# Kernel tuning notes

Measured on AMD Instinct MI355X. Metric: run time of the kernel, lower is better.

The kernel has to match this reference:

```python
import jax, jax.numpy as jnp
import numpy as np

M, N, P, T = 8000, 63, 64, 5


def setup_inputs() -> dict:
    key = jax.random.key(0)
    ks = jax.random.split(key, 19)
    sn = (1.0 / N) ** 0.5
    sp = (1.0 / P) ** 0.5
    f32 = jnp.float32
    return {
        "A": jax.random.normal(ks[0], (1, M, N), f32),
        "b": jax.random.normal(ks[1], (1, M), f32),
        "c": jax.random.normal(ks[2], (1, N), f32),
        "theta1r": sn * jax.random.normal(ks[3], (P, N + 1), f32),
        "theta1c": sn * jax.random.normal(ks[4], (P, N + 1), f32),
        "theta2rr": sp * jax.random.normal(ks[5], (P, P), f32),
        "theta2rc": sp * jax.random.normal(ks[6], (P, P), f32),
        "theta2cr": sp * jax.random.normal(ks[7], (P, P), f32),
        "theta3rr": sp * jax.random.normal(ks[8], (P, P), f32),
        "theta3rc": sp * jax.random.normal(ks[9], (P, P), f32),
        "theta3cr": sp * jax.random.normal(ks[10], (P, P), f32),
        "theta4rr": sp * jax.random.normal(ks[11], (P,), f32),
        "theta4rc": sp * jax.random.normal(ks[12], (P,), f32),
        "theta4cr": sp * jax.random.normal(ks[13], (P,), f32),
        "theta6r": sp * jax.random.normal(ks[14], (P, P), f32),
        "theta6c": sp * jax.random.normal(ks[15], (P, P), f32),
        "theta7": sp * jax.random.normal(ks[16], (P, P), f32),
        "W8": 0.05 * jax.random.normal(ks[17], (2, 2 * P), f32),
        "b8": 0.05 * jax.random.normal(ks[18], (2,), f32),
        "z": 7,
    }


def reference(A, b, c, theta1r, theta1c, theta2rr, theta2rc, theta2cr,
              theta3rr, theta3rc, theta3cr, theta4rr, theta4rc, theta4cr,
              theta6r, theta6c, theta7, W8, b8, z):
    relu = jax.nn.relu
    m, n = A.shape[1], A.shape[2]
    p = theta1r.shape[0]
    # raw node features: row node v -> [A[v,:], b[v]]; column node m -> [c, 0]
    Fr_raw = jnp.concatenate([A[0], b[0][:, None]], axis=1)        # (m, n+1)
    fc_raw = jnp.concatenate([c[0], jnp.zeros((1,), A.dtype)])     # (n+1,)
    Fr = Fr_raw / jnp.linalg.norm(Fr_raw, axis=1, keepdims=True)   # f(v), v < m
    fc = fc_raw / jnp.linalg.norm(fc_raw)                          # f(m)
    # edge weights w(v,u) = f(v).f(u) are detached in the original (float(...data))
    Frd = jax.lax.stop_gradient(Fr)
    fcd = jax.lax.stop_gradient(fc)
    Wrr = Frd @ Frd.T                                              # (m, m)
    dg = jnp.diagonal(Wrr)
    srr_pos = relu(Wrr).sum(axis=1) - relu(dg)                     # sum over u != v
    srr_neg = relu(-Wrr).sum(axis=1) - relu(-dg)
    wrc = Frd @ fcd                                                # (m,) = w(v, m)
    # identity: sum_u relu(t4 * w_u) = relu(t4) * sum_u relu(w_u) + relu(-t4) * sum_u relu(-w_u)
    Srr = relu(theta4rr)[:, None] * srr_pos[None, :] + relu(-theta4rr)[:, None] * srr_neg[None, :]
    Src = relu(theta4rc)[:, None] * relu(wrc)[None, :] + relu(-theta4rc)[:, None] * relu(-wrc)[None, :]
    scr = relu(theta4cr) * relu(wrc).sum() + relu(-theta4cr) * relu(-wrc).sum()
    edge_r = theta3rr @ Srr + theta3rc @ Src                       # (p, m), constant over t
    edge_c = theta3cr @ scr                                        # (p,)
    fz = Fr[z]                                                     # z < m: row node feature
    t1r = theta1r @ fz                                             # (p,)
    t1c = theta1c @ fz
    # mu init (p, m+1) = [[Ab^T, c0^T]; 0]; split into row columns / column node
    mu_r0 = jnp.zeros((p, m), A.dtype).at[: n + 1].set(Fr_raw.T)
    mu_c0 = jnp.zeros((p,), A.dtype).at[: n + 1].set(fc_raw)

    def step(carry, _):
        mu_r, mu_c = carry
        # row nodes: term2rr uses old mu[:, v]; term2rc uses old mu[:, m]
        new_r = relu(t1r[:, None] + theta2rr @ mu_r + (theta2rc @ mu_c)[:, None] + edge_r)
        # column node updated last within a sweep -> sees updated row embeddings
        new_c = relu(t1c + theta2cr @ new_r.sum(axis=1) + edge_c)
        return (new_r, new_c), None

    (mu_r, mu_c), _ = jax.lax.scan(step, (mu_r0, mu_c0), None, length=T)
    term6 = theta6r @ mu_r.sum(axis=1) + theta6c @ mu_c            # (p,)
    term7 = theta7 @ mu_r[:, z]                                    # (p,)
    feat = jax.nn.sigmoid(jnp.concatenate([term6, term7]))         # (2p,)
    return (feat @ W8.T + b8)[None, :]                             # (1, 2)
```

## Files before the change

### kernel.cpp

```cpp
#include <hip/hip_runtime.h>
#include <math.h>

typedef __attribute__((ext_vector_type(8))) short short8;
typedef __attribute__((ext_vector_type(4))) float f32x4;

#define WS_SPART 0
#define WS_GPART 131072
#define WS_WPART 163840
#define WS_CPART 164864
#define WS_T1R   204864
#define WS_T1C   204928
#define WS_AL    204992
#define WS_BE    205056
#define WS_GA    205120
#define WS_DE    205184
#define WS_ECP   205248
#define WS_ECN   205312
#define WS_W     205376
#define WS_MUZ   205760
#define WS_WSUM  205824
#define WS_RNORM 205888
#define WS_R2H   214080
#define WS_R2L   216128
#define WS_E4    218176
#define WS_FH    250176
#define WS_FL    512320

__device__ __forceinline__ float waveReduceSum(float v) {
#pragma unroll
    for (int m = 32; m >= 1; m >>= 1) v += __shfl_xor(v, m, 64);
    return v;
}
__device__ __forceinline__ unsigned short f2bf(float f) {
    unsigned int u = __float_as_uint(f);
    unsigned int r = (u + 0x7fffu + ((u >> 16) & 1u)) >> 16;
    return (unsigned short)r;
}
__device__ __forceinline__ float bf2f(unsigned short h) {
    return __uint_as_float(((unsigned int)h) << 16);
}

__global__ __launch_bounds__(256) void k_fr(
    const float* __restrict__ A, const float* __restrict__ b, const float* __restrict__ c,
    const float* __restrict__ th1r, const float* __restrict__ th1c,
    const float* __restrict__ th2rr, const float* __restrict__ th2rc,
    const float* __restrict__ th3rr, const float* __restrict__ th3rc, const float* __restrict__ th3cr,
    const float* __restrict__ th4rr, const float* __restrict__ th4rc, const float* __restrict__ th4cr,
    const int* __restrict__ zp,
    unsigned short* __restrict__ Fh, unsigned short* __restrict__ Fl,
    unsigned short* __restrict__ R2H, unsigned short* __restrict__ R2L,
    float* __restrict__ ws)
{
    int tid = threadIdx.x, lane = tid & 63, wid = tid >> 6;

    if (blockIdx.x == 512) {
        __shared__ float fcraw[64], fz[64], sh4a[64], sh4b[64];
        int p = lane;
        int z = zp[0];
        float cv = (p < 63) ? c[p] : 0.f;
        fcraw[p] = cv;
        float av = (p < 63) ? A[z * 63 + p] : b[z];
        float s2 = waveReduceSum(av * av);
        fz[p] = av * rsqrtf(s2);
        __syncthreads();

        float t1 = 0.f, t2 = 0.f, w0 = 0.f;
#pragma unroll 8
        for (int k = 0; k < 64; k++) {
            t1 += th1r[p * 64 + k] * fz[k];
            t2 += th1c[p * 64 + k] * fz[k];
            w0 += th2rc[p * 64 + k] * fcraw[k];
        }
        ws[WS_T1R + p] = t1;
        ws[WS_T1C + p] = t2;
        ws[WS_W + p] = t1 + w0;

        sh4a[p] = th4rr[p];
        sh4b[p] = th4rc[p];
        __syncthreads();
        float a = 0.f, bb = 0.f, g = 0.f, d = 0.f;
#pragma unroll 8
        for (int k = 0; k < 64; k++) {
            float t4 = sh4a[k];
            a  += th3rr[p * 64 + k] * fmaxf(t4, 0.f);
            bb += th3rr[p * 64 + k] * fmaxf(-t4, 0.f);
            float t5 = sh4b[k];
            g  += th3rc[p * 64 + k] * fmaxf(t5, 0.f);
            d  += th3rc[p * 64 + k] * fmaxf(-t5, 0.f);
        }
        ws[WS_AL + p] = a; ws[WS_BE + p] = bb;
        ws[WS_GA + p] = g; ws[WS_DE + p] = d;
        __syncthreads();
        sh4a[p] = th4cr[p];
        __syncthreads();
        float e1 = 0.f, e2 = 0.f;
#pragma unroll 8
        for (int k = 0; k < 64; k++) {
            float t6 = sh4a[k];
            e1 += th3cr[p * 64 + k] * fmaxf(t6, 0.f);
            e2 += th3cr[p * 64 + k] * fmaxf(-t6, 0.f);
        }
        ws[WS_ECP + p] = e1; ws[WS_ECN + p] = e2;

#pragma unroll
        for (int i = 0; i < 16; i++) {
            int idx = tid * 16 + i;
            float f = th2rr[idx];
            unsigned short h = f2bf(f);
            R2H[idx] = h;
            R2L[idx] = f2bf(f - bf2f(h));
        }
        return;
    }

    __shared__ float gsh[64];
    __shared__ float wsh2[2];
    if (tid < 64) gsh[tid] = 0.f;
    if (tid < 2) wsh2[tid] = 0.f;
    __syncthreads();

    float cv = (lane < 63) ? c[lane] : 0.f;
    float cn2 = waveReduceSum(cv * cv);
    float fcnl = cv * rsqrtf(cn2);

    int r0 = blockIdx.x * 16 + wid * 4;
    float gl = 0.f, lp = 0.f, ln = 0.f;
#pragma unroll
    for (int i = 0; i < 4; i++) {
        int r = r0 + i;
        if (r < 8000) {
            float val = (lane < 63) ? A[r * 63 + lane] : b[r];
            float s2 = waveReduceSum(val * val);
            float f = val * rsqrtf(s2);
            unsigned short h = f2bf(f);
            Fh[r * 64 + lane] = h;
            Fl[r * 64 + lane] = f2bf(f - bf2f(h));
            gl += f;
            float w = waveReduceSum(f * fcnl);
            if (lane == 0) {
                ws[WS_RNORM + r] = sqrtf(s2);
                lp += fmaxf(w, 0.f); ln += fmaxf(-w, 0.f);
            }
        } else {
            Fh[r * 64 + lane] = 0;
            Fl[r * 64 + lane] = 0;
        }
    }
    atomicAdd(&gsh[lane], gl);
    if (lane == 0) { atomicAdd(&wsh2[0], lp); atomicAdd(&wsh2[1], ln); }
    __syncthreads();
    if (tid < 64) ws[WS_GPART + blockIdx.x * 64 + tid] = gsh[tid];
    if (tid == 64) ws[WS_WPART + blockIdx.x * 2 + 0] = wsh2[0];
    if (tid == 65) ws[WS_WPART + blockIdx.x * 2 + 1] = wsh2[1];
}

__global__ __launch_bounds__(256) void k_gram(
    const unsigned short* __restrict__ Fh, const unsigned short* __restrict__ Fl,
    float* __restrict__ ws)
{
    __shared__ short BshH[2][16 * 72];
    __shared__ short BshL[2][16 * 72];
    int tid = threadIdx.x, lane = tid & 63, wid = tid >> 6;
    int m = lane & 15, quad = lane >> 4;
    int vbase = blockIdx.x * 256 + wid * 64;
    int sr = tid >> 4, sc = (tid & 15) * 4;

    short8 AH[8], AL[8];
#pragma unroll
    for (int pt = 0; pt < 4; pt++)
#pragma unroll
        for (int q = 0; q < 2; q++) {
            int off = (vbase + pt * 16 + m) * 64 + q * 32 + quad * 8;
            AH[pt * 2 + q] = *(const short8*)(Fh + off);
            AL[pt * 2 + q] = *(const short8*)(Fl + off);
        }
    float srr[16];
#pragma unroll
    for (int i = 0; i < 16; i++) srr[i] = 0.f;

    const int y = blockIdx.y;
    {
        int u0 = y * 16;
        *(uint2*)(&BshH[0][sr * 72 + sc]) = *(const uint2*)(Fh + (u0 + sr) * 64 + sc);
        *(uint2*)(&BshL[0][sr * 72 + sc]) = *(const uint2*)(Fl + (u0 + sr) * 64 + sc);
    }
    __syncthreads();

#pragma unroll 1
    for (int k = 0; k < 32; k++) {
        int cur = k & 1;
        uint2 sH, sL;
        if (k < 31) {
            int u0 = (y + 16 * (k + 1)) * 16;
            sH = *(const uint2*)(Fh + (u0 + sr) * 64 + sc);
            sL = *(const uint2*)(Fl + (u0 + sr) * 64 + sc);
        }
        short8 BH[2], BL[2];
#pragma unroll
        for (int q = 0; q < 2; q++) {
            BH[q] = *(const short8*)(&BshH[cur][m * 72 + q * 32 + quad * 8]);
            BL[q] = *(const short8*)(&BshL[cur][m * 72 + q * 32 + quad * 8]);
        }
#pragma unroll
        for (int pt = 0; pt < 4; pt++) {
            f32x4 a = {0.f, 0.f, 0.f, 0.f};
#pragma unroll
            for (int q = 0; q < 2; q++) {
                a = __builtin_amdgcn_mfma_f32_16x16x32_bf16(AH[pt*2+q], BH[q], a, 0, 0, 0);
                a = __builtin_amdgcn_mfma_f32_16x16x32_bf16(AH[pt*2+q], BL[q], a, 0, 0, 0);
                a = __builtin_amdgcn_mfma_f32_16x16x32_bf16(AL[pt*2+q], BH[q], a, 0, 0, 0);
            }
#pragma unroll
            for (int r = 0; r < 4; r++) srr[pt*4+r] += fmaxf(a[r], 0.f);
        }
        if (k < 31) {
            *(uint2*)(&BshH[1 - cur][sr * 72 + sc]) = sH;
            *(uint2*)(&BshL[1 - cur][sr * 72 + sc]) = sL;
            __syncthreads();
        }
    }
#pragma unroll
    for (int pt = 0; pt < 4; pt++)
#pragma unroll
        for (int r = 0; r < 4; r++) {
            float s = srr[pt * 4 + r];
#pragma unroll
            for (int mm = 8; mm >= 1; mm >>= 1) s += __shfl_xor(s, mm, 64);
            if (m == 0)
                ws[WS_SPART + y * 8192 + vbase + pt * 16 + quad * 4 + r] = s;
        }
}

__global__ __launch_bounds__(256) void k_e4(
    const float* __restrict__ c, float* __restrict__ ws,
    unsigned short* __restrict__ MH, unsigned short* __restrict__ ML)
{
    __shared__ float fcnS[64], gS[64], sprow[64], red[256];
    int tid = threadIdx.x, lane = tid & 63, wid = tid >> 6;

    float cv = (lane < 63) ? c[lane] : 0.f;
    float cn2 = waveReduceSum(cv * cv);
    if (wid == 0) fcnS[lane] = cv * rsqrtf(cn2);

    float gv = 0.f;
    for (int bb = 0; bb < 128; bb++) gv += ws[WS_GPART + (wid * 128 + bb) * 64 + lane];
    red[tid] = gv;
    __syncthreads();
    if (tid < 64) gS[tid] = red[tid] + red[64 + tid] + red[128 + tid] + red[192 + tid];
    if (wid == 1) {
        float wp = 0.f;
#pragma unroll
        for (int k = 0; k < 8; k++) wp += ws[WS_WPART + (lane + 64 * k) * 2];
        wp = waveReduceSum(wp);
        if (lane == 0) ws[WS_WSUM] = wp;
    }
    if (wid == 2) {
        float wn = 0.f;
#pragma unroll
        for (int k = 0; k < 8; k++) wn += ws[WS_WPART + (lane + 64 * k) * 2 + 1];
        wn = waveReduceSum(wn);
        if (lane == 0) ws[WS_WSUM + 1] = wn;
    }
    int v0 = blockIdx.x * 64;
    float sv = 0.f;
#pragma unroll
    for (int y = wid * 4; y < wid * 4 + 4; y++) sv += ws[WS_SPART + y * 8192 + v0 + lane];
    __syncthreads();
    red[tid] = sv;
    __syncthreads();
    if (tid < 64) sprow[tid] = red[tid] + red[64 + tid] + red[128 + tid] + red[192 + tid];
    __syncthreads();

    for (int i2 = 0; i2 < 16; i2++) {
        int i = wid * 16 + i2;
        int v = v0 + i;
        float fr = bf2f(MH[v * 64 + lane]) + bf2f(ML[v * 64 + lane]);
        float dw = waveReduceSum(fr * fcnS[lane]);
        float dg = waveReduceSum(fr * gS[lane]);
        if (lane == 0) {
            float spv = sprow[i];
            float4 e;
            e.x = spv - 1.0f;
            e.y = spv - dg;
            e.z = fmaxf(dw, 0.f);
            e.w = fmaxf(-dw, 0.f);
            *(float4*)(ws + WS_E4 + v * 4) = e;
        }
        float x = fr * ws[WS_RNORM + v];
        unsigned short h = f2bf(x);
        MH[v * 64 + lane] = h;
        ML[v * 64 + lane] = f2bf(x - bf2f(h));
    }
}

__global__ __launch_bounds__(256) void k_mu(
    const int* __restrict__ zp, float* __restrict__ ws,
    unsigned short* __restrict__ MH, unsigned short* __restrict__ ML,
    const unsigned short* __restrict__ R2H, const unsigned short* __restrict__ R2L,
    int t)
{
    __shared__ __align__(16) float wS[64], alS[64], beS[64], gaS[64], deS[64];
    __shared__ float colp[256];
    int tid = threadIdx.x, lane = tid & 63, wid = tid >> 6;
    int m = lane & 15, quad = lane >> 4;
    int v = (blockIdx.x * 4 + wid) * 16 + m;
    int z = zp[0];

    if (wid == 0) wS[lane] = ws[WS_W + t * 64 + lane];
    else if (wid == 1) { alS[lane] = ws[WS_AL + lane]; beS[lane] = ws[WS_BE + lane]; }
    else if (wid == 2) { gaS[lane] = ws[WS_GA + lane]; deS[lane] = ws[WS_DE + lane]; }

    short8 RH[8], RL[8];
#pragma unroll
    for (int pt = 0; pt < 4; pt++)
#pragma unroll
        for (int q = 0; q < 2; q++) {
            int off = (pt * 16 + m) * 64 + q * 32 + quad * 8;
            RH[pt * 2 + q] = *(const short8*)(R2H + off);
            RL[pt * 2 + q] = *(const short8*)(R2L + off);
        }
    short8 BH[2], BL[2];
#pragma unroll
    for (int q = 0; q < 2; q++) {
        BH[q] = *(const short8*)(MH + v * 64 + q * 32 + quad * 8);
        BL[q] = *(const short8*)(ML + v * 64 + q * 32 + quad * 8);
    }
    float4 e = *(const float4*)(ws + WS_E4 + v * 4);
    __syncthreads();

#pragma unroll
    for (int pt = 0; pt < 4; pt++) {
        f32x4 a = {0.f, 0.f, 0.f, 0.f};
#pragma unroll
        for (int q = 0; q < 2; q++) {
            a = __builtin_amdgcn_mfma_f32_16x16x32_bf16(RH[pt*2+q], BH[q], a, 0, 0, 0);
            a = __builtin_amdgcn_mfma_f32_16x16x32_bf16(RH[pt*2+q], BL[q], a, 0, 0, 0);
            a = __builtin_amdgcn_mfma_f32_16x16x32_bf16(RL[pt*2+q], BH[q], a, 0, 0, 0);
        }
        int pbase = pt * 16 + quad * 4;
        float4 w4 = *(const float4*)(wS + pbase);
        float4 a4 = *(const float4*)(alS + pbase);
        float4 b4 = *(const float4*)(beS + pbase);
        float4 g4 = *(const float4*)(gaS + pbase);
        float4 d4 = *(const float4*)(deS + pbase);
        float u0 = fmaxf(a[0] + w4.x + a4.x*e.x + b4.x*e.y + g4.x*e.z + d4.x*e.w, 0.f);
        float u1 = fmaxf(a[1] + w4.y + a4.y*e.x + b4.y*e.y + g4.y*e.z + d4.y*e.w, 0.f);
        float u2 = fmaxf(a[2] + w4.z + a4.z*e.x + b4.z*e.y + g4.z*e.z + d4.z*e.w, 0.f);
        float u3 = fmaxf(a[3] + w4.w + a4.w*e.x + b4.w*e.y + g4.w*e.z + d4.w*e.w, 0.f);
        ushort4 h4, l4;
        h4.x = f2bf(u0); l4.x = f2bf(u0 - bf2f(h4.x));
        h4.y = f2bf(u1); l4.y = f2bf(u1 - bf2f(h4.y));
        h4.z = f2bf(u2); l4.z = f2bf(u2 - bf2f(h4.z));
        h4.w = f2bf(u3); l4.w = f2bf(u3 - bf2f(h4.w));
        *(ushort4*)(MH + v * 64 + pbase) = h4;
        *(ushort4*)(ML + v * 64 + pbase) = l4;
        float c0 = u0, c1 = u1, c2 = u2, c3 = u3;
#pragma unroll
        for (int mm = 1; mm < 16; mm <<= 1) {
            c0 += __shfl_xor(c0, mm, 64);
            c1 += __shfl_xor(c1, mm, 64);
            c2 += __shfl_xor(c2, mm, 64);
            c3 += __shfl_xor(c3, mm, 64);
        }
        if (m == 0) {
            colp[wid * 64 + pbase + 0] = c0;
            colp[wid * 64 + pbase + 1] = c1;
            colp[wid * 64 + pbase + 2] = c2;
            colp[wid * 64 + pbase + 3] = c3;
        }
        if (t == 4 && v == z) {
            float4 o; o.x = u0; o.y = u1; o.z = u2; o.w = u3;
            *(float4*)(ws + WS_MUZ + pbase) = o;
        }
    }
    __syncthreads();
    if (tid < 64)
        ws[WS_CPART + t * 8000 + blockIdx.x * 64 + tid] =
            colp[tid] + colp[64 + tid] + colp[128 + tid] + colp[192 + tid];
}

__global__ __launch_bounds__(256) void k_colup(
    const float* __restrict__ th2cr, const float* __restrict__ th2rc,
    const float* __restrict__ th6r, const float* __restrict__ th6c,
    const float* __restrict__ th7, const float* __restrict__ W8,
    const float* __restrict__ b8,
    float* __restrict__ ws, float* __restrict__ out, int t)
{
    __shared__ float red[256], Ssh[64], ysh[64], wsh[64], feat[128];
    int tid = threadIdx.x, lane = tid & 63, wid = tid >> 6;
    int m = lane & 15, quad = lane >> 4;

    float s = 0.f;
    for (int blk = wid; blk < 125; blk += 4)
        s += ws[WS_CPART + t * 8000 + blk * 64 + lane];
    red[tid] = s;
    __syncthreads();
    if (tid < 64) Ssh[tid] = red[tid] + red[64 + tid] + red[128 + tid] + red[192 + tid];
    __syncthreads();
    {
        int p = wid * 16 + m;
        float acc = 0.f;
        const float4* rowp = (const float4*)(th2cr + p * 64 + quad * 16);
#pragma unroll
        for (int kk = 0; kk < 4; kk++) {
            float4 r4 = rowp[kk];
            acc += r4.x * Ssh[quad * 16 + 4 * kk]     + r4.y * Ssh[quad * 16 + 4 * kk + 1]
                 + r4.z * Ssh[quad * 16 + 4 * kk + 2] + r4.w * Ssh[quad * 16 + 4 * kk + 3];
        }
        acc += __shfl_xor(acc, 16, 64);
        acc += __shfl_xor(acc, 32, 64);
        if (quad == 0)
            ysh[p] = fmaxf(acc + ws[WS_T1C + p] + ws[WS_WSUM] * ws[WS_ECP + p]
                           + ws[WS_WSUM + 1] * ws[WS_ECN + p], 0.f);
    }
    __syncthreads();
    {
        int p = wid * 16 + m;
        float acc = 0.f;
        const float4* rowp = (const float4*)(th2rc + p * 64 + quad * 16);
#pragma unroll
        for (int kk = 0; kk < 4; kk++) {
            float4 r4 = rowp[kk];
            acc += r4.x * ysh[quad * 16 + 4 * kk]     + r4.y * ysh[quad * 16 + 4 * kk + 1]
                 + r4.z * ysh[quad * 16 + 4 * kk + 2] + r4.w * ysh[quad * 16 + 4 * kk + 3];
        }
        acc += __shfl_xor(acc, 16, 64);
        acc += __shfl_xor(acc, 32, 64);
        if (quad == 0) wsh[p] = acc + ws[WS_T1R + p];
    }
    __syncthreads();
    if (tid < 64) ws[WS_W + (t + 1) * 64 + tid] = wsh[tid];

    if (t == 4) {
        int p = tid;
        if (p < 64) {
            float t6 = 0.f, t7 = 0.f;
#pragma unroll 8
            for (int k = 0; k < 64; k++) {
                t6 += th6r[p * 64 + k] * Ssh[k] + th6c[p * 64 + k] * ysh[k];
                t7 += th7[p * 64 + k] * ws[WS_MUZ + k];
            }
            feat[p] = 1.f / (1.f + expf(-t6));
            feat[64 + p] = 1.f / (1.f + expf(-t7));
        }
        __syncthreads();
        if (p < 2) {
            float o = b8[p];
            for (int i = 0; i < 128; i++) o += W8[p * 128 + i] * feat[i];
            out[p] = o;
        }
    }
}

extern "C" void kernel_launch(void* const* d_in, const int* in_sizes, int n_in,
                              void* d_out, int out_size, void* d_ws, size_t ws_size,
                              hipStream_t stream) {
    (void)in_sizes; (void)n_in; (void)out_size; (void)ws_size;
    const float* A     = (const float*)d_in[0];
    const float* b     = (const float*)d_in[1];
    const float* c     = (const float*)d_in[2];
    const float* th1r  = (const float*)d_in[3];
    const float* th1c  = (const float*)d_in[4];
    const float* th2rr = (const float*)d_in[5];
    const float* th2rc = (const float*)d_in[6];
    const float* th2cr = (const float*)d_in[7];
    const float* th3rr = (const float*)d_in[8];
    const float* th3rc = (const float*)d_in[9];
    const float* th3cr = (const float*)d_in[10];
    const float* th4rr = (const float*)d_in[11];
    const float* th4rc = (const float*)d_in[12];
    const float* th4cr = (const float*)d_in[13];
    const float* th6r  = (const float*)d_in[14];
    const float* th6c  = (const float*)d_in[15];
    const float* th7   = (const float*)d_in[16];
    const float* W8    = (const float*)d_in[17];
    const float* b8    = (const float*)d_in[18];
    const int*   zp    = (const int*)d_in[19];
    float* ws  = (float*)d_ws;
    float* out = (float*)d_out;
    unsigned short* Fh  = (unsigned short*)(ws + WS_FH);
    unsigned short* Fl  = (unsigned short*)(ws + WS_FL);
    unsigned short* R2H = (unsigned short*)(ws + WS_R2H);
    unsigned short* R2L = (unsigned short*)(ws + WS_R2L);

    k_fr<<<513, 256, 0, stream>>>(A, b, c, th1r, th1c, th2rr, th2rc, th3rr, th3rc,
                                  th3cr, th4rr, th4rc, th4cr, zp, Fh, Fl, R2H, R2L, ws);
    k_gram<<<dim3(32, 16), 256, 0, stream>>>(Fh, Fl, ws);
    k_e4<<<125, 256, 0, stream>>>(c, ws, Fh, Fl);
    for (int t = 0; t < 5; t++) {
        k_mu<<<125, 256, 0, stream>>>(zp, ws, Fh, Fl, R2H, R2L, t);
        k_colup<<<1, 256, 0, stream>>>(th2cr, th2rc, th6r, th6c, th7, W8, b8, ws, out, t);
    }
}
```

Measured before the change: 239.0 us.

## Use hi-only bf16 Gram and fuse first mu step into e4 kernel

The Gram kernel now uses only the high bf16 half of the features, cutting MFMA count from three to one per product and halving B-tile loads. Each tile is also widened to 32 columns, which halves the loop trip count. The e4 setup kernel is merged with the first mu iteration, so normalized features go straight through LDS into the MFMA update and one launch plus a global round trip disappear. Dropping the low-half correction lowers the precision of the relu-summed edge weights, which risks accuracy drift.

```diff
diff --git a/kernel.cpp b/kernel.cpp
--- a/kernel.cpp
+++ b/kernel.cpp
@@ -155,67 +155,55 @@
 }
 
 __global__ __launch_bounds__(256) void k_gram(
-    const unsigned short* __restrict__ Fh, const unsigned short* __restrict__ Fl,
-    float* __restrict__ ws)
+    const unsigned short* __restrict__ Fh, float* __restrict__ ws)
 {
-    __shared__ short BshH[2][16 * 72];
-    __shared__ short BshL[2][16 * 72];
+    __shared__ short Bsh[2][32 * 72];
     int tid = threadIdx.x, lane = tid & 63, wid = tid >> 6;
     int m = lane & 15, quad = lane >> 4;
     int vbase = blockIdx.x * 256 + wid * 64;
-    int sr = tid >> 4, sc = (tid & 15) * 4;
-
-    short8 AH[8], AL[8];
+    int srow = tid >> 3;
+    int scol = (tid & 7) * 8;
+
+    short8 AH[8];
 #pragma unroll
     for (int pt = 0; pt < 4; pt++)
 #pragma unroll
-        for (int q = 0; q < 2; q++) {
-            int off = (vbase + pt * 16 + m) * 64 + q * 32 + quad * 8;
-            AH[pt * 2 + q] = *(const short8*)(Fh + off);
-            AL[pt * 2 + q] = *(const short8*)(Fl + off);
-        }
+        for (int q = 0; q < 2; q++)
+            AH[pt * 2 + q] = *(const short8*)(Fh + (vbase + pt * 16 + m) * 64 + q * 32 + quad * 8);
+
     float srr[16];
 #pragma unroll
     for (int i = 0; i < 16; i++) srr[i] = 0.f;
 
     const int y = blockIdx.y;
-    {
-        int u0 = y * 16;
-        *(uint2*)(&BshH[0][sr * 72 + sc]) = *(const uint2*)(Fh + (u0 + sr) * 64 + sc);
-        *(uint2*)(&BshL[0][sr * 72 + sc]) = *(const uint2*)(Fl + (u0 + sr) * 64 + sc);
-    }
+    *(short8*)(&Bsh[0][srow * 72 + scol]) = *(const short8*)(Fh + (y * 32 + srow) * 64 + scol);
     __syncthreads();
 
 #pragma unroll 1
-    for (int k = 0; k < 32; k++) {
+    for (int k = 0; k < 16; k++) {
         int cur = k & 1;
-        uint2 sH, sL;
-        if (k < 31) {
-            int u0 = (y + 16 * (k + 1)) * 16;
-            sH = *(const uint2*)(Fh + (u0 + sr) * 64 + sc);
-            sL = *(const uint2*)(Fl + (u0 + sr) * 64 + sc);
-        }
-        short8 BH[2], BL[2];
-#pragma unroll
-        for (int q = 0; q < 2; q++) {
-            BH[q] = *(const short8*)(&BshH[cur][m * 72 + q * 32 + quad * 8]);
-            BL[q] = *(const short8*)(&BshL[cur][m * 72 + q * 32 + quad * 8]);
-        }
-#pragma unroll
-        for (int pt = 0; pt < 4; pt++) {
-            f32x4 a = {0.f, 0.f, 0.f, 0.f};
-#pragma unroll
-            for (int q = 0; q < 2; q++) {
-                a = __builtin_amdgcn_mfma_f32_16x16x32_bf16(AH[pt*2+q], BH[q], a, 0, 0, 0);
-                a = __builtin_amdgcn_mfma_f32_16x16x32_bf16(AH[pt*2+q], BL[q], a, 0, 0, 0);
-                a = __builtin_amdgcn_mfma_f32_16x16x32_bf16(AL[pt*2+q], BH[q], a, 0, 0, 0);
+        short8 pre;
+        if (k < 15) {
+            int cch = y + 16 * (k + 1);
+            pre = *(const short8*)(Fh + (cch * 32 + srow) * 64 + scol);
+        }
+#pragma unroll
+        for (int s = 0; s < 2; s++) {
+            short8 BH[2];
+#pragma unroll
+            for (int q = 0; q < 2; q++)
+                BH[q] = *(const short8*)(&Bsh[cur][(s * 16 + m) * 72 + q * 32 + quad * 8]);
+#pragma unroll
+            for (int pt = 0; pt < 4; pt++) {
+                f32x4 a = {0.f, 0.f, 0.f, 0.f};
+                a = __builtin_amdgcn_mfma_f32_16x16x32_bf16(AH[pt * 2 + 0], BH[0], a, 0, 0, 0);
+                a = __builtin_amdgcn_mfma_f32_16x16x32_bf16(AH[pt * 2 + 1], BH[1], a, 0, 0, 0);
+#pragma unroll
+                for (int r = 0; r < 4; r++) srr[pt * 4 + r] += fmaxf(a[r], 0.f);
             }
-#pragma unroll
-            for (int r = 0; r < 4; r++) srr[pt*4+r] += fmaxf(a[r], 0.f);
-        }
-        if (k < 31) {
-            *(uint2*)(&BshH[1 - cur][sr * 72 + sc]) = sH;
-            *(uint2*)(&BshL[1 - cur][sr * 72 + sc]) = sL;
+        }
+        if (k < 15) {
+            *(short8*)(&Bsh[1 - cur][srow * 72 + scol]) = pre;
             __syncthreads();
         }
     }
@@ -224,48 +212,59 @@
 #pragma unroll
         for (int r = 0; r < 4; r++) {
             float s = srr[pt * 4 + r];
-#pragma unroll
-            for (int mm = 8; mm >= 1; mm >>= 1) s += __shfl_xor(s, mm, 64);
+            s += __shfl_xor(s, 1, 64); s += __shfl_xor(s, 2, 64);
+            s += __shfl_xor(s, 4, 64); s += __shfl_xor(s, 8, 64);
             if (m == 0)
                 ws[WS_SPART + y * 8192 + vbase + pt * 16 + quad * 4 + r] = s;
         }
 }
 
-__global__ __launch_bounds__(256) void k_e4(
+__global__ __launch_bounds__(256) void k_mu0(
     const float* __restrict__ c, float* __restrict__ ws,
-    unsigned short* __restrict__ MH, unsigned short* __restrict__ ML)
+    unsigned short* __restrict__ MH, unsigned short* __restrict__ ML,
+    const unsigned short* __restrict__ R2H, const unsigned short* __restrict__ R2L)
 {
-    __shared__ float fcnS[64], gS[64], sprow[64], red[256];
+    __shared__ float XF[64][68];
+    __shared__ float red[256], colp[256];
+    __shared__ __align__(16) float wS[64], alS[64], beS[64], gaS[64], deS[64];
+    __shared__ float fcnS[64], gS[64], sprow[64];
+    __shared__ __align__(16) float e4sh[256];
     int tid = threadIdx.x, lane = tid & 63, wid = tid >> 6;
-
-    float cv = (lane < 63) ? c[lane] : 0.f;
-    float cn2 = waveReduceSum(cv * cv);
-    if (wid == 0) fcnS[lane] = cv * rsqrtf(cn2);
-
-    float gv = 0.f;
-    for (int bb = 0; bb < 128; bb++) gv += ws[WS_GPART + (wid * 128 + bb) * 64 + lane];
-    red[tid] = gv;
-    __syncthreads();
-    if (tid < 64) gS[tid] = red[tid] + red[64 + tid] + red[128 + tid] + red[192 + tid];
-    if (wid == 1) {
+    int m = lane & 15, quad = lane >> 4;
+    int v0 = blockIdx.x * 64;
+    int cw = wid * 16 + m;
+    int v = v0 + cw;
+
+    if (wid == 0) {
+        float cv = (lane < 63) ? c[lane] : 0.f;
+        float cn2 = waveReduceSum(cv * cv);
+        fcnS[lane] = cv * rsqrtf(cn2);
+        wS[lane] = ws[WS_W + lane];
+    } else if (wid == 1) {
+        alS[lane] = ws[WS_AL + lane]; beS[lane] = ws[WS_BE + lane];
         float wp = 0.f;
 #pragma unroll
         for (int k = 0; k < 8; k++) wp += ws[WS_WPART + (lane + 64 * k) * 2];
         wp = waveReduceSum(wp);
         if (lane == 0) ws[WS_WSUM] = wp;
-    }
-    if (wid == 2) {
+    } else if (wid == 2) {
+        gaS[lane] = ws[WS_GA + lane]; deS[lane] = ws[WS_DE + lane];
         float wn = 0.f;
 #pragma unroll
         for (int k = 0; k < 8; k++) wn += ws[WS_WPART + (lane + 64 * k) * 2 + 1];
         wn = waveReduceSum(wn);
         if (lane == 0) ws[WS_WSUM + 1] = wn;
     }
-    int v0 = blockIdx.x * 64;
+    float gv = 0.f;
+#pragma unroll 8
+    for (int bb = 0; bb < 128; bb++) gv += ws[WS_GPART + (wid * 128 + bb) * 64 + lane];
+    red[tid] = gv;
+    __syncthreads();
+    if (tid < 64) gS[tid] = red[tid] + red[64 + tid] + red[128 + tid] + red[192 + tid];
+    __syncthreads();
     float sv = 0.f;
 #pragma unroll
     for (int y = wid * 4; y < wid * 4 + 4; y++) sv += ws[WS_SPART + y * 8192 + v0 + lane];
-    __syncthreads();
     red[tid] = sv;
     __syncthreads();
     if (tid < 64) sprow[tid] = red[tid] + red[64 + tid] + red[128 + tid] + red[192 + tid];
@@ -273,8 +272,8 @@
 
     for (int i2 = 0; i2 < 16; i2++) {
         int i = wid * 16 + i2;
-        int v = v0 + i;
-        float fr = bf2f(MH[v * 64 + lane]) + bf2f(ML[v * 64 + lane]);
+        int vr = v0 + i;
+        float fr = bf2f(MH[vr * 64 + lane]) + bf2f(ML[vr * 64 + lane]);
         float dw = waveReduceSum(fr * fcnS[lane]);
         float dg = waveReduceSum(fr * gS[lane]);
         if (lane == 0) {
@@ -284,13 +283,85 @@
             e.y = spv - dg;
             e.z = fmaxf(dw, 0.f);
             e.w = fmaxf(-dw, 0.f);
-            *(float4*)(ws + WS_E4 + v * 4) = e;
-        }
-        float x = fr * ws[WS_RNORM + v];
-        unsigned short h = f2bf(x);
-        MH[v * 64 + lane] = h;
-        ML[v * 64 + lane] = f2bf(x - bf2f(h));
-    }
+            *(float4*)(&e4sh[i * 4]) = e;
+            *(float4*)(ws + WS_E4 + vr * 4) = e;
+        }
+        XF[i][lane] = fr * ws[WS_RNORM + vr];
+    }
+
+    short8 RH[8], RL[8];
+#pragma unroll
+    for (int pt = 0; pt < 4; pt++)
+#pragma unroll
+        for (int q = 0; q < 2; q++) {
+            int off = (pt * 16 + m) * 64 + q * 32 + quad * 8;
+            RH[pt * 2 + q] = *(const short8*)(R2H + off);
+            RL[pt * 2 + q] = *(const short8*)(R2L + off);
+        }
+    __syncthreads();
+
+    short8 BH[2], BL[2];
+#pragma unroll
+    for (int q = 0; q < 2; q++) {
+        float4 f0 = *(const float4*)(&XF[cw][q * 32 + quad * 8]);
+        float4 f1 = *(const float4*)(&XF[cw][q * 32 + quad * 8 + 4]);
+        float xv[8] = {f0.x, f0.y, f0.z, f0.w, f1.x, f1.y, f1.z, f1.w};
+        short8 H, L;
+#pragma unroll
+        for (int j = 0; j < 8; j++) {
+            unsigned short h = f2bf(xv[j]);
+            H[j] = (short)h;
+            L[j] = (short)f2bf(xv[j] - bf2f(h));
+        }
+        BH[q] = H; BL[q] = L;
+    }
+    float4 e = *(const float4*)(&e4sh[cw * 4]);
+
+#pragma unroll
+    for (int pt = 0; pt < 4; pt++) {
+        f32x4 a = {0.f, 0.f, 0.f, 0.f};
+#pragma unroll
+        for (int q = 0; q < 2; q++) {
+            a = __builtin_amdgcn_mfma_f32_16x16x32_bf16(RH[pt*2+q], BH[q], a, 0, 0, 0);
+            a = __builtin_amdgcn_mfma_f32_16x16x32_bf16(RH[pt*2+q], BL[q], a, 0, 0, 0);
+            a = __builtin_amdgcn_mfma_f32_16x16x32_bf16(RL[pt*2+q], BH[q], a, 0, 0, 0);
+        }
+        int pbase = pt * 16 + quad * 4;
+        float4 w4 = *(const float4*)(wS + pbase);
+        float4 a4 = *(const float4*)(alS + pbase);
+        float4 b4 = *(const float4*)(beS + pbase);
+        float4 g4 = *(const float4*)(gaS + pbase);
+        float4 d4 = *(const float4*)(deS + pbase);
+        float u0 = fmaxf(a[0] + w4.x + a4.x*e.x + b4.x*e.y + g4.x*e.z + d4.x*e.w, 0.f);
+        float u1 = fmaxf(a[1] + w4.y + a4.y*e.x + b4.y*e.y + g4.y*e.z + d4.y*e.w, 0.f);
+        float u2 = fmaxf(a[2] + w4.z + a4.z*e.x + b4.z*e.y + g4.z*e.z + d4.z*e.w, 0.f);
+        float u3 = fmaxf(a[3] + w4.w + a4.w*e.x + b4.w*e.y + g4.w*e.z + d4.w*e.w, 0.f);
+        ushort4 h4, l4;
+        h4.x = f2bf(u0); l4.x = f2bf(u0 - bf2f(h4.x));
+        h4.y = f2bf(u1); l4.y = f2bf(u1 - bf2f(h4.y));
+        h4.z = f2bf(u2); l4.z = f2bf(u2 - bf2f(h4.z));
+        h4.w = f2bf(u3); l4.w = f2bf(u3 - bf2f(h4.w));
+        *(ushort4*)(MH + v * 64 + pbase) = h4;
+        *(ushort4*)(ML + v * 64 + pbase) = l4;
+        float c0 = u0, c1 = u1, c2 = u2, c3 = u3;
+#pragma unroll
+        for (int mm = 1; mm < 16; mm <<= 1) {
+            c0 += __shfl_xor(c0, mm, 64);
+            c1 += __shfl_xor(c1, mm, 64);
+            c2 += __shfl_xor(c2, mm, 64);
+            c3 += __shfl_xor(c3, mm, 64);
+        }
+        if (m == 0) {
+            colp[wid * 64 + pbase + 0] = c0;
+            colp[wid * 64 + pbase + 1] = c1;
+            colp[wid * 64 + pbase + 2] = c2;
+            colp[wid * 64 + pbase + 3] = c3;
+        }
+    }
+    __syncthreads();
+    if (tid < 64)
+        ws[WS_CPART + blockIdx.x * 64 + tid] =
+            colp[tid] + colp[64 + tid] + colp[128 + tid] + colp[192 + tid];
 }
 
 __global__ __launch_bounds__(256) void k_mu(
@@ -485,10 +556,11 @@
 
     k_fr<<<513, 256, 0, stream>>>(A, b, c, th1r, th1c, th2rr, th2rc, th3rr, th3rc,
                                   th3cr, th4rr, th4rc, th4cr, zp, Fh, Fl, R2H, R2L, ws);
-    k_gram<<<dim3(32, 16), 256, 0, stream>>>(Fh, Fl, ws);
-    k_e4<<<125, 256, 0, stream>>>(c, ws, Fh, Fl);
+    k_gram<<<dim3(32, 16), 256, 0, stream>>>(Fh, ws);
+    k_mu0<<<125, 256, 0, stream>>>(c, ws, Fh, Fl, R2H, R2L);
     for (int t = 0; t < 5; t++) {
-        k_mu<<<125, 256, 0, stream>>>(zp, ws, Fh, Fl, R2H, R2L, t);
         k_colup<<<1, 256, 0, stream>>>(th2cr, th2rc, th6r, th6c, th7, W8, b8, ws, out, t);
-    }
-}
+        if (t < 4)
+            k_mu<<<125, 256, 0, stream>>>(zp, ws, Fh, Fl, R2H, R2L, t + 1);
+    }
+}
```

Result: faster. 224.3 us (-6.1%).
